# Kernel optimization log

Measured on AMD Instinct MI355X. Metric: run time of the kernel, lower is better.

## Reference

```python
import jax, jax.numpy as jnp
import numpy as np

B, C, H, W = 512, 64, 32, 64
NUM_NODE = 128


def setup_inputs() -> dict:
    key = jax.random.key(0)
    ks = jax.random.split(key, 11)
    f = jnp.float32
    def nrm(k, shape, s):
        return jax.random.normal(k, shape, f) * s
    return {
        "x":   jax.random.normal(ks[0], (B, C, H, W), f),
        "w11": nrm(ks[1], (32, 64, 1, 1), 0.1), "b11": nrm(ks[2], (32,), 0.05),
        "w12": nrm(ks[3], (16, 32, 3, 3), 0.1), "b12": nrm(ks[4], (16,), 0.05),
        "w21": nrm(ks[5], (8, 16, 1, 1), 0.1),  "b21": nrm(ks[6], (8,), 0.05),
        "w22": nrm(ks[7], (4, 8, 3, 3), 0.1),   "b22": nrm(ks[8], (4,), 0.05),
        "fcw": nrm(ks[9], (2 * NUM_NODE, 32 * 64 * 4), 0.05),
        "fcb": nrm(ks[10], (2 * NUM_NODE,), 0.05),
    }


def _conv_relu(x, w, b, pad):
    y = jax.lax.conv_general_dilated(
        x, w, window_strides=(1, 1), padding=[(pad, pad), (pad, pad)],
        dimension_numbers=("NCHW", "OIHW", "NCHW"))
    return jax.nn.relu(y + b[None, :, None, None])


def reference(x, w11, b11, w12, b12, w21, b21, w22, b22, fcw, fcb):
    # --- GraphGen3: conv stack -> fc -> n_Sigmoid -> [B, N, 2] ---
    h = _conv_relu(x, w11, b11, 0)
    h = _conv_relu(h, w12, b12, 1)
    h = _conv_relu(h, w21, b21, 0)
    h = _conv_relu(h, w22, b22, 1)          # [B, 4, 32, 64]
    z = h.reshape(h.shape[0], -1) @ fcw.T + fcb  # [B, 2N]
    c01 = jax.nn.sigmoid(3.0 * z).reshape(x.shape[0], -1, 2)  # n_Sigmoid(x, 3)
    # --- get_coord: scale normalized coords to pixel range ---
    Hd, Wd = x.shape[2], x.shape[3]
    coord = c01 * jnp.array([Hd - 1, Wd - 1], x.dtype)  # [B, N, 2]
    # --- th_batch_map_coordinates: clamp, corner gather, bilinear lerp ---
    ch = jnp.clip(coord[..., 0], 0.0, Hd - 1)
    cw = jnp.clip(coord[..., 1], 0.0, Wd - 1)
    h0 = jnp.floor(ch).astype(jnp.int32); h1 = jnp.ceil(ch).astype(jnp.int32)
    w0 = jnp.floor(cw).astype(jnp.int32); w1 = jnp.ceil(cw).astype(jnp.int32)
    bidx = jnp.arange(x.shape[0])[:, None]  # [B, 1]
    def gv(hi, wi):
        return x[bidx, :, hi, wi]           # gather -> [B, N, C]
    v_lt = gv(h0, w0); v_rt = gv(h1, w0)
    v_lb = gv(h0, w1); v_rb = gv(h1, w1)
    oh = (ch - h0.astype(x.dtype))[..., None]
    ow = (cw - w0.astype(x.dtype))[..., None]
    vt = v_lt + oh * (v_rt - v_lt)
    vb = v_lb + oh * (v_rb - v_lb)
    graph_feat = vt + ow * (vb - vt)        # [B, N, C] (matches permute(0,2,1))
    return graph_feat, coord
```

## Files before the change

kernel.cpp:

```cpp
#include <hip/hip_runtime.h>
#include <cstdint>

#define BATCH 512
#define CIN   64
#define HH    32
#define WW    64
#define HW    2048
#define C1    32
#define C2    16
#define C3    8
#define C4    4
#define NOUT  256
#define KFC   8192
#define NODES 128
#define KS    16
#define GF_SIZE (BATCH * NODES * CIN)

typedef __attribute__((ext_vector_type(8))) short bfrag;
typedef __attribute__((ext_vector_type(4))) float ffrag;

__device__ __forceinline__ ushort bf_trunc(float f) { return (ushort)(__float_as_uint(f) >> 16); }
__device__ __forceinline__ float  bf_truncf(float f) { return __uint_as_float(__float_as_uint(f) & 0xffff0000u); }
__device__ __forceinline__ ushort f2bf(float f) {
  uint32_t u = __float_as_uint(f);
  return (ushort)((u + 0x7fffu + ((u >> 16) & 1u)) >> 16);
}
__device__ __forceinline__ uint32_t pack2(float a, float b) {
  return (uint32_t)f2bf(a) | ((uint32_t)f2bf(b) << 16);
}
__device__ __forceinline__ uint32_t packhi2(float a, float b) {
  return (uint32_t)bf_trunc(a) | ((uint32_t)bf_trunc(b) << 16);
}

__global__ __launch_bounds__(256) void k_conv12(
    const float* __restrict__ x, const float* __restrict__ w11, const float* __restrict__ b11,
    const float* __restrict__ w12, const float* __restrict__ b12,
    float* __restrict__ h2, int b0)
{
  __shared__ __align__(16) char h1s[10 * 66 * 64];
  const int tid = threadIdx.x;
  const int l   = tid & 63;
  const int wv  = tid >> 6;
  const int lr  = l & 15;
  const int lg  = l >> 4;
  const int r0  = blockIdx.x * 8;
  const int bg  = b0 + blockIdx.y;
  const float* xb = x + (size_t)bg * CIN * HW;

  if (tid < 160) {
    int row = tid >> 4, half = (tid >> 3) & 1, q = tid & 7;
    int cell = row * 66 + (half ? 65 : 0);
    *(uint2*)(h1s + (cell << 6) + q * 8) = uint2{0u, 0u};
  }

  bfrag w1h[2][2], w1l[2][2];
  #pragma unroll
  for (int m = 0; m < 2; ++m) {
    #pragma unroll
    for (int ks = 0; ks < 2; ++ks) {
      const float* wp = w11 + (m * 16 + lr) * 64 + ks * 32 + lg * 8;
      #pragma unroll
      for (int e = 0; e < 8; ++e) {
        float v = wp[e];
        w1h[m][ks][e] = (short)bf_trunc(v);
        w1l[m][ks][e] = (short)f2bf(v - bf_truncf(v));
      }
    }
  }
  float bias1[2][4];
  #pragma unroll
  for (int m = 0; m < 2; ++m) {
    #pragma unroll
    for (int r = 0; r < 4; ++r) bias1[m][r] = b11[m * 16 + lg * 4 + r];
  }

  #pragma unroll 2
  for (int i = 0; i < 10; ++i) {
    const int nt   = wv * 10 + i;
    const int ry   = nt >> 2;
    const int col0 = (nt & 3) << 4;
    const int y    = r0 - 1 + ry;
    const int colb = col0 + 1 + lr;
    if (y >= 0 && y < HH) {
      const float* xp = xb + y * WW + col0 + lr;
      bfrag xh[2];
      #pragma unroll
      for (int ks = 0; ks < 2; ++ks) {
        #pragma unroll
        for (int e = 0; e < 8; ++e)
          xh[ks][e] = (short)f2bf(xp[(ks * 32 + lg * 8 + e) * HW]);
      }
      ffrag a0 = {0.f, 0.f, 0.f, 0.f}, a1 = {0.f, 0.f, 0.f, 0.f};
      #pragma unroll
      for (int ks = 0; ks < 2; ++ks) {
        a0 = __builtin_amdgcn_mfma_f32_16x16x32_bf16(w1h[0][ks], xh[ks], a0, 0, 0, 0);
        a0 = __builtin_amdgcn_mfma_f32_16x16x32_bf16(w1l[0][ks], xh[ks], a0, 0, 0, 0);
        a1 = __builtin_amdgcn_mfma_f32_16x16x32_bf16(w1h[1][ks], xh[ks], a1, 0, 0, 0);
        a1 = __builtin_amdgcn_mfma_f32_16x16x32_bf16(w1l[1][ks], xh[ks], a1, 0, 0, 0);
      }
      #pragma unroll
      for (int m = 0; m < 2; ++m) {
        float v0 = fmaxf((m ? a1[0] : a0[0]) + bias1[m][0], 0.f);
        float v1 = fmaxf((m ? a1[1] : a0[1]) + bias1[m][1], 0.f);
        float v2 = fmaxf((m ? a1[2] : a0[2]) + bias1[m][2], 0.f);
        float v3 = fmaxf((m ? a1[3] : a0[3]) + bias1[m][3], 0.f);
        int chunk = (m * 2 + (lg >> 1)) ^ ((colb >> 1) & 3);
        char* dst = h1s + ((ry * 66 + colb) << 6) + (chunk << 4) + (lg & 1) * 8;
        *(uint2*)dst = uint2{pack2(v0, v1), pack2(v2, v3)};
      }
    } else {
      #pragma unroll
      for (int m = 0; m < 2; ++m) {
        int chunk = (m * 2 + (lg >> 1)) ^ ((colb >> 1) & 3);
        char* dst = h1s + ((ry * 66 + colb) << 6) + (chunk << 4) + (lg & 1) * 8;
        *(uint2*)dst = uint2{0u, 0u};
      }
    }
  }
  __syncthreads();

  bfrag w2h[9], w2l[9];
  #pragma unroll
  for (int t = 0; t < 9; ++t) {
    const float* wp = w12 + lr * 288 + t;
    #pragma unroll
    for (int e = 0; e < 8; ++e) {
      float v = wp[(lg * 8 + e) * 9];
      w2h[t][e] = (short)bf_trunc(v);
      w2l[t][e] = (short)f2bf(v - bf_truncf(v));
    }
  }
  float bias2[4];
  #pragma unroll
  for (int r = 0; r < 4; ++r) bias2[r] = b12[lg * 4 + r];

  #pragma unroll 2
  for (int i = 0; i < 8; ++i) {
    const int nt   = wv * 8 + i;
    const int ryo  = nt >> 2;
    const int col0 = (nt & 3) << 4;
    ffrag acc = {0.f, 0.f, 0.f, 0.f};
    #pragma unroll
    for (int ky = 0; ky < 3; ++ky) {
      const int row = ryo + ky;
      #pragma unroll
      for (int kx = 0; kx < 3; ++kx) {
        const int colb  = col0 + lr + kx;
        const int chunk = lg ^ ((colb >> 1) & 3);
        const bfrag hv = *(const bfrag*)(h1s + ((row * 66 + colb) << 6) + (chunk << 4));
        acc = __builtin_amdgcn_mfma_f32_16x16x32_bf16(w2h[ky * 3 + kx], hv, acc, 0, 0, 0);
        acc = __builtin_amdgcn_mfma_f32_16x16x32_bf16(w2l[ky * 3 + kx], hv, acc, 0, 0, 0);
      }
    }
    const int px = (r0 + ryo) * WW + col0 + lr;
    float4 o;
    o.x = fmaxf(acc[0] + bias2[0], 0.f);
    o.y = fmaxf(acc[1] + bias2[1], 0.f);
    o.z = fmaxf(acc[2] + bias2[2], 0.f);
    o.w = fmaxf(acc[3] + bias2[3], 0.f);
    *(float4*)(h2 + ((size_t)blockIdx.y * HW + px) * 16 + lg * 4) = o;
  }
}

__global__ __launch_bounds__(256) void k_conv34(
    const float* __restrict__ h2, const float* __restrict__ w21, const float* __restrict__ b21,
    const float* __restrict__ w22, const float* __restrict__ b22,
    ushort* __restrict__ h4h, ushort* __restrict__ h4l)
{
  __shared__ float h3s[18][64][9];
  __shared__ float __align__(16) w21s[128];
  __shared__ float __align__(16) w22s[288];
  const int tid = threadIdx.x;
  const int r0  = blockIdx.x * 16;
  const size_t b = blockIdx.y;

  for (int i = tid; i < 128; i += 256) w21s[(i & 15) * 8 + (i >> 4)] = w21[i];
  for (int i = tid; i < 288; i += 256) {
    int o = i / 72, r = i - o * 72, c = r / 9, tap = r - c * 9;
    w22s[(tap * 8 + c) * 4 + o] = w22[i];
  }
  __syncthreads();

  for (int p = tid; p < 18 * 64; p += 256) {
    const int ry = p >> 6, wc = p & 63;
    const int y  = r0 - 1 + ry;
    float* hd = &h3s[ry][wc][0];
    if (y >= 0 && y < HH) {
      const float4* hp = (const float4*)(h2 + ((b * HH + y) * WW + wc) * C2);
      float4 v0 = hp[0], v1 = hp[1], v2 = hp[2], v3 = hp[3];
      float xv[16] = {v0.x, v0.y, v0.z, v0.w, v1.x, v1.y, v1.z, v1.w,
                      v2.x, v2.y, v2.z, v2.w, v3.x, v3.y, v3.z, v3.w};
      float acc[C3];
      #pragma unroll
      for (int o = 0; o < C3; ++o) acc[o] = b21[o];
      #pragma unroll
      for (int c = 0; c < 16; ++c) {
        const float4* wr = (const float4*)&w21s[c * 8];
        float4 a = wr[0], d = wr[1];
        float v = xv[c];
        acc[0] = fmaf(v, a.x, acc[0]); acc[1] = fmaf(v, a.y, acc[1]);
        acc[2] = fmaf(v, a.z, acc[2]); acc[3] = fmaf(v, a.w, acc[3]);
        acc[4] = fmaf(v, d.x, acc[4]); acc[5] = fmaf(v, d.y, acc[5]);
        acc[6] = fmaf(v, d.z, acc[6]); acc[7] = fmaf(v, d.w, acc[7]);
      }
      #pragma unroll
      for (int c = 0; c < C3; ++c) hd[c] = fmaxf(acc[c], 0.f);
    } else {
      #pragma unroll
      for (int c = 0; c < C3; ++c) hd[c] = 0.f;
    }
  }
  __syncthreads();

  for (int p = tid; p < 1024; p += 256) {
    const int yl = p >> 6, wc = p & 63, ry = yl + 1;
    float acc[C4] = {b22[0], b22[1], b22[2], b22[3]};
    #pragma unroll
    for (int ky = 0; ky < 3; ++ky) {
      #pragma unroll
      for (int kx = 0; kx < 3; ++kx) {
        const int wcc = wc + kx - 1;
        if (wcc < 0 || wcc >= WW) continue;
        const float* hb = &h3s[ry + ky - 1][wcc][0];
        const int tap = ky * 3 + kx;
        #pragma unroll
        for (int c = 0; c < C3; ++c) {
          float v = hb[c];
          float4 w4 = *(const float4*)&w22s[(tap * 8 + c) * 4];
          acc[0] = fmaf(v, w4.x, acc[0]); acc[1] = fmaf(v, w4.y, acc[1]);
          acc[2] = fmaf(v, w4.z, acc[2]); acc[3] = fmaf(v, w4.w, acc[3]);
        }
      }
    }
    const size_t base = b * KFC + (r0 + yl) * WW + wc;
    #pragma unroll
    for (int o = 0; o < C4; ++o) {
      float v = fmaxf(acc[o], 0.f);
      h4h[base + (size_t)o * HW] = bf_trunc(v);
      h4l[base + (size_t)o * HW] = f2bf(v - bf_truncf(v));
    }
  }
}

__global__ __launch_bounds__(256) void k_cvt_fcw(
    const float* __restrict__ w, ushort* __restrict__ hi, ushort* __restrict__ lo)
{
  const int i = (blockIdx.x * 256 + threadIdx.x) * 8;
  const float4 a = *(const float4*)(w + i);
  const float4 b = *(const float4*)(w + i + 4);
  uint4 hv, lv;
  hv.x = packhi2(a.x, a.y); hv.y = packhi2(a.z, a.w);
  hv.z = packhi2(b.x, b.y); hv.w = packhi2(b.z, b.w);
  lv.x = pack2(a.x - bf_truncf(a.x), a.y - bf_truncf(a.y));
  lv.y = pack2(a.z - bf_truncf(a.z), a.w - bf_truncf(a.w));
  lv.z = pack2(b.x - bf_truncf(b.x), b.y - bf_truncf(b.y));
  lv.w = pack2(b.z - bf_truncf(b.z), b.w - bf_truncf(b.w));
  *(uint4*)(hi + i) = hv;
  *(uint4*)(lo + i) = lv;
}

__global__ __launch_bounds__(256) void k_fc(
    const ushort* __restrict__ Ahp, const ushort* __restrict__ Alp,
    const ushort* __restrict__ Bhp, const ushort* __restrict__ Blp,
    float* __restrict__ zpart, int cb)
{
  const int tid = threadIdx.x;
  const int l   = tid & 63;
  const int wv  = tid >> 6;
  const int lr  = l & 15;
  const int lg  = l >> 4;
  const int m0  = blockIdx.x * 64 + (wv >> 1) * 32;
  const int n0  = blockIdx.y * 64 + (wv & 1) * 32;
  const int k0  = blockIdx.z * (KFC / KS);

  int mrow[2], nrow[2];
  #pragma unroll
  for (int t = 0; t < 2; ++t) {
    int m = m0 + t * 16 + lr;
    mrow[t] = m < cb ? m : cb - 1;
    nrow[t] = n0 + t * 16 + lr;
  }
  ffrag acc[2][2] = {};

  #pragma unroll 1
  for (int kc = 0; kc < (KFC / KS) / 32; ++kc) {
    const int k = k0 + kc * 32 + lg * 8;
    bfrag ah[2], al[2], bh[2], bl[2];
    #pragma unroll
    for (int t = 0; t < 2; ++t) {
      ah[t] = *(const bfrag*)(Ahp + (size_t)mrow[t] * KFC + k);
      al[t] = *(const bfrag*)(Alp + (size_t)mrow[t] * KFC + k);
      bh[t] = *(const bfrag*)(Bhp + (size_t)nrow[t] * KFC + k);
      bl[t] = *(const bfrag*)(Blp + (size_t)nrow[t] * KFC + k);
    }
    #pragma unroll
    for (int mt = 0; mt < 2; ++mt) {
      #pragma unroll
      for (int nt = 0; nt < 2; ++nt) {
        acc[mt][nt] = __builtin_amdgcn_mfma_f32_16x16x32_bf16(ah[mt], bh[nt], acc[mt][nt], 0, 0, 0);
        acc[mt][nt] = __builtin_amdgcn_mfma_f32_16x16x32_bf16(ah[mt], bl[nt], acc[mt][nt], 0, 0, 0);
        acc[mt][nt] = __builtin_amdgcn_mfma_f32_16x16x32_bf16(al[mt], bh[nt], acc[mt][nt], 0, 0, 0);
      }
    }
  }

  #pragma unroll
  for (int mt = 0; mt < 2; ++mt) {
    #pragma unroll
    for (int r = 0; r < 4; ++r) {
      const int m = m0 + mt * 16 + lg * 4 + r;
      if (m < cb) {
        #pragma unroll
        for (int nt = 0; nt < 2; ++nt)
          zpart[((size_t)blockIdx.z * cb + m) * NOUT + n0 + nt * 16 + lr] = acc[mt][nt][r];
      }
    }
  }
}

__global__ __launch_bounds__(256) void k_gather(
    const float* __restrict__ x, const float* __restrict__ zpart,
    const float* __restrict__ fcb, float* __restrict__ out, int cb, int b0)
{
  const int bid = blockIdx.x;
  int bl, g;
  if ((cb & 7) == 0) {
    const int xcd = bid & 7;
    const int j   = bid >> 3;
    g  = j & 31;
    bl = (j >> 5) * 8 + xcd;
  } else {
    bl = bid >> 5;
    g  = bid & 31;
  }
  const int node = g * 4 + (threadIdx.x >> 6);
  const int l    = threadIdx.x & 63;
  const int bg   = b0 + bl;

  float val = 0.f;
  if (l < 2 * KS) {
    const int kb = l >> 1, comp = l & 1;
    val = zpart[((size_t)kb * cb + bl) * NOUT + node * 2 + comp];
  }
  #pragma unroll
  for (int off = 2; off < 2 * KS; off <<= 1) val += __shfl_xor(val, off);
  const float z0 = __shfl(val, 0) + fcb[node * 2 + 0];
  const float z1 = __shfl(val, 1) + fcb[node * 2 + 1];
  const float ch = 31.f / (1.f + __expf(-3.f * z0));
  const float cw = 63.f / (1.f + __expf(-3.f * z1));

  if (l < 2)
    out[GF_SIZE + (((size_t)bg * NODES + node) << 1) + l] = l ? cw : ch;

  const float chv = fminf(fmaxf(ch, 0.f), 31.f);
  const float cwv = fminf(fmaxf(cw, 0.f), 63.f);
  const float fh = floorf(chv), fw = floorf(cwv);
  const int h0 = (int)fh, h1i = (int)ceilf(chv);
  const int w0 = (int)fw, w1i = (int)ceilf(cwv);
  const float oh = chv - fh, ow = cwv - fw;
  const float* xb = x + ((size_t)bg * CIN + l) * HW;
  const float v_lt = xb[h0 * WW + w0];
  const float v_rt = xb[h1i * WW + w0];
  const float v_lb = xb[h0 * WW + w1i];
  const float v_rb = xb[h1i * WW + w1i];
  const float vt = v_lt + oh * (v_rt - v_lt);
  const float vb = v_lb + oh * (v_rb - v_lb);
  out[((size_t)bg * NODES + node) * CIN + l] = vt + ow * (vb - vt);
}

extern "C" void kernel_launch(void* const* d_in, const int* in_sizes, int n_in,
                              void* d_out, int out_size, void* d_ws, size_t ws_size,
                              hipStream_t stream)
{
  (void)in_sizes; (void)n_in; (void)out_size;
  const float* x   = (const float*)d_in[0];
  const float* w11 = (const float*)d_in[1];
  const float* b11 = (const float*)d_in[2];
  const float* w12 = (const float*)d_in[3];
  const float* b12 = (const float*)d_in[4];
  const float* w21 = (const float*)d_in[5];
  const float* b21 = (const float*)d_in[6];
  const float* w22 = (const float*)d_in[7];
  const float* b22 = (const float*)d_in[8];
  const float* fcw = (const float*)d_in[9];
  const float* fcb = (const float*)d_in[10];
  float* out = (float*)d_out;
  char* wsb  = (char*)d_ws;

  const size_t perB  = 131072 + 16384 + 16384 + (size_t)KS * NOUT * 4;
  const size_t fixed = 2 * 4194304;
  size_t avail = ws_size > fixed ? ws_size - fixed : perB;
  size_t cbmax = avail / perB;
  int CB = (int)(cbmax < (size_t)BATCH ? cbmax : (size_t)BATCH);
  if (CB < 1) CB = 1;

  char* p = wsb;
  float*  h2v  = (float*)p;   p += (size_t)CB * 131072;
  ushort* h4h  = (ushort*)p;  p += (size_t)CB * 16384;
  ushort* h4l  = (ushort*)p;  p += (size_t)CB * 16384;
  float*  zpv  = (float*)p;   p += (size_t)CB * KS * NOUT * 4;
  ushort* fcwh = (ushort*)p;  p += 4194304;
  ushort* fcwl = (ushort*)p;

  k_cvt_fcw<<<dim3(NOUT * KFC / (256 * 8)), 256, 0, stream>>>(fcw, fcwh, fcwl);

  for (int b0 = 0; b0 < BATCH; b0 += CB) {
    const int cb = (BATCH - b0 < CB) ? (BATCH - b0) : CB;
    k_conv12<<<dim3(4, cb), 256, 0, stream>>>(x, w11, b11, w12, b12, h2v, b0);
    k_conv34<<<dim3(2, cb), 256, 0, stream>>>(h2v, w21, b21, w22, b22, h4h, h4l);
    k_fc<<<dim3((cb + 63) / 64, 4, KS), 256, 0, stream>>>(h4h, h4l, fcwh, fcwl, zpv, cb);
    k_gather<<<dim3(cb * 32), 256, 0, stream>>>(x, zpv, fcb, out, cb, b0);
  }
}
```

Baseline: 263.1 us.

## Store conv2 output as fp16, halve conv12 row tile, prefetch input tiles

```diff
diff --git a/kernel.cpp b/kernel.cpp
--- a/kernel.cpp
+++ b/kernel.cpp
@@ -1,4 +1,5 @@
 #include <hip/hip_runtime.h>
+#include <hip/hip_fp16.h>
 #include <cstdint>
 
 #define BATCH 512
@@ -31,26 +32,31 @@
 __device__ __forceinline__ uint32_t packhi2(float a, float b) {
   return (uint32_t)bf_trunc(a) | ((uint32_t)bf_trunc(b) << 16);
 }
-
-__global__ __launch_bounds__(256) void k_conv12(
+__device__ __forceinline__ ushort f2h(float f) { return __half_as_ushort(__float2half_rn(f)); }
+__device__ __forceinline__ uint32_t packh2(float a, float b) {
+  return (uint32_t)f2h(a) | ((uint32_t)f2h(b) << 16);
+}
+__device__ __forceinline__ float h2f(uint32_t u) { return __half2float(__ushort_as_half((ushort)u)); }
+
+__global__ __launch_bounds__(256, 5) void k_conv12(
     const float* __restrict__ x, const float* __restrict__ w11, const float* __restrict__ b11,
     const float* __restrict__ w12, const float* __restrict__ b12,
-    float* __restrict__ h2, int b0)
-{
-  __shared__ __align__(16) char h1s[10 * 66 * 64];
+    ushort* __restrict__ h2, int b0)
+{
+  __shared__ __align__(16) char h1s[6 * 66 * 64];
   const int tid = threadIdx.x;
   const int l   = tid & 63;
   const int wv  = tid >> 6;
   const int lr  = l & 15;
   const int lg  = l >> 4;
-  const int r0  = blockIdx.x * 8;
+  const int r0  = blockIdx.x * 4;
   const int bg  = b0 + blockIdx.y;
   const float* xb = x + (size_t)bg * CIN * HW;
 
-  if (tid < 160) {
-    int row = tid >> 4, half = (tid >> 3) & 1, q = tid & 7;
-    int cell = row * 66 + (half ? 65 : 0);
-    *(uint2*)(h1s + (cell << 6) + q * 8) = uint2{0u, 0u};
+  if (tid < 96) {
+    int cell = tid >> 3, q = tid & 7;
+    int row = cell >> 1, colb = (cell & 1) ? 65 : 0;
+    *(uint2*)(h1s + ((row * 66 + colb) << 6) + q * 8) = uint2{0u, 0u};
   }
 
   bfrag w1h[2][2], w1l[2][2];
@@ -74,96 +80,122 @@
     for (int r = 0; r < 4; ++r) bias1[m][r] = b11[m * 16 + lg * 4 + r];
   }
 
-  #pragma unroll 2
-  for (int i = 0; i < 10; ++i) {
-    const int nt   = wv * 10 + i;
-    const int ry   = nt >> 2;
-    const int col0 = (nt & 3) << 4;
-    const int y    = r0 - 1 + ry;
-    const int colb = col0 + 1 + lr;
+  float bufA[16], bufB[16];
+
+  auto loadx16 = [&](int nt, float (&buf)[16]) {
+    const int ry = nt >> 2, col0 = (nt & 3) << 4;
+    const int y  = r0 - 1 + ry;
     if (y >= 0 && y < HH) {
       const float* xp = xb + y * WW + col0 + lr;
-      bfrag xh[2];
-      #pragma unroll
-      for (int ks = 0; ks < 2; ++ks) {
+      #pragma unroll
+      for (int ks = 0; ks < 2; ++ks)
         #pragma unroll
         for (int e = 0; e < 8; ++e)
-          xh[ks][e] = (short)f2bf(xp[(ks * 32 + lg * 8 + e) * HW]);
-      }
-      ffrag a0 = {0.f, 0.f, 0.f, 0.f}, a1 = {0.f, 0.f, 0.f, 0.f};
-      #pragma unroll
-      for (int ks = 0; ks < 2; ++ks) {
-        a0 = __builtin_amdgcn_mfma_f32_16x16x32_bf16(w1h[0][ks], xh[ks], a0, 0, 0, 0);
-        a0 = __builtin_amdgcn_mfma_f32_16x16x32_bf16(w1l[0][ks], xh[ks], a0, 0, 0, 0);
-        a1 = __builtin_amdgcn_mfma_f32_16x16x32_bf16(w1h[1][ks], xh[ks], a1, 0, 0, 0);
-        a1 = __builtin_amdgcn_mfma_f32_16x16x32_bf16(w1l[1][ks], xh[ks], a1, 0, 0, 0);
-      }
-      #pragma unroll
-      for (int m = 0; m < 2; ++m) {
+          buf[ks * 8 + e] = xp[(ks * 32 + lg * 8 + e) * HW];
+    } else {
+      #pragma unroll
+      for (int j = 0; j < 16; ++j) buf[j] = 0.f;
+    }
+  };
+
+  auto comp_tile = [&](int nt, const float (&buf)[16]) {
+    const int ry = nt >> 2, col0 = (nt & 3) << 4;
+    const int y  = r0 - 1 + ry;
+    const bool valid = (y >= 0) && (y < HH);
+    const int colb = col0 + 1 + lr;
+    bfrag xh[2];
+    #pragma unroll
+    for (int ks = 0; ks < 2; ++ks)
+      #pragma unroll
+      for (int e = 0; e < 8; ++e)
+        xh[ks][e] = (short)f2bf(buf[ks * 8 + e]);
+    ffrag a0 = {0.f, 0.f, 0.f, 0.f}, a1 = {0.f, 0.f, 0.f, 0.f};
+    #pragma unroll
+    for (int ks = 0; ks < 2; ++ks) {
+      a0 = __builtin_amdgcn_mfma_f32_16x16x32_bf16(w1h[0][ks], xh[ks], a0, 0, 0, 0);
+      a0 = __builtin_amdgcn_mfma_f32_16x16x32_bf16(w1l[0][ks], xh[ks], a0, 0, 0, 0);
+      a1 = __builtin_amdgcn_mfma_f32_16x16x32_bf16(w1h[1][ks], xh[ks], a1, 0, 0, 0);
+      a1 = __builtin_amdgcn_mfma_f32_16x16x32_bf16(w1l[1][ks], xh[ks], a1, 0, 0, 0);
+    }
+    #pragma unroll
+    for (int m = 0; m < 2; ++m) {
+      uint2 sv;
+      if (valid) {
         float v0 = fmaxf((m ? a1[0] : a0[0]) + bias1[m][0], 0.f);
         float v1 = fmaxf((m ? a1[1] : a0[1]) + bias1[m][1], 0.f);
         float v2 = fmaxf((m ? a1[2] : a0[2]) + bias1[m][2], 0.f);
         float v3 = fmaxf((m ? a1[3] : a0[3]) + bias1[m][3], 0.f);
-        int chunk = (m * 2 + (lg >> 1)) ^ ((colb >> 1) & 3);
-        char* dst = h1s + ((ry * 66 + colb) << 6) + (chunk << 4) + (lg & 1) * 8;
-        *(uint2*)dst = uint2{pack2(v0, v1), pack2(v2, v3)};
-      }
-    } else {
-      #pragma unroll
-      for (int m = 0; m < 2; ++m) {
-        int chunk = (m * 2 + (lg >> 1)) ^ ((colb >> 1) & 3);
-        char* dst = h1s + ((ry * 66 + colb) << 6) + (chunk << 4) + (lg & 1) * 8;
-        *(uint2*)dst = uint2{0u, 0u};
-      }
-    }
+        sv = uint2{pack2(v0, v1), pack2(v2, v3)};
+      } else {
+        sv = uint2{0u, 0u};
+      }
+      int chunk = (m * 2 + (lg >> 1)) ^ ((colb >> 1) & 3);
+      char* dst = h1s + ((ry * 66 + colb) << 6) + (chunk << 4) + (lg & 1) * 8;
+      *(uint2*)dst = sv;
+    }
+  };
+
+  loadx16(wv * 6 + 0, bufA);
+  #pragma unroll
+  for (int i = 0; i < 6; ++i) {
+    if (i < 5) loadx16(wv * 6 + i + 1, (i & 1) ? bufA : bufB);
+    if (i & 1) comp_tile(wv * 6 + i, bufB);
+    else       comp_tile(wv * 6 + i, bufA);
   }
   __syncthreads();
 
-  bfrag w2h[9], w2l[9];
-  #pragma unroll
-  for (int t = 0; t < 9; ++t) {
-    const float* wp = w12 + lr * 288 + t;
-    #pragma unroll
-    for (int e = 0; e < 8; ++e) {
-      float v = wp[(lg * 8 + e) * 9];
-      w2h[t][e] = (short)bf_trunc(v);
-      w2l[t][e] = (short)f2bf(v - bf_truncf(v));
+  ffrag acc2[4] = {{0.f,0.f,0.f,0.f},{0.f,0.f,0.f,0.f},{0.f,0.f,0.f,0.f},{0.f,0.f,0.f,0.f}};
+  #pragma unroll
+  for (int pass = 0; pass < 2; ++pass) {
+    const int t0 = pass ? 5 : 0;
+    const int tn = pass ? 4 : 5;
+    bfrag wh[5], wl[5];
+    #pragma unroll
+    for (int tt = 0; tt < 5; ++tt) {
+      if (tt < tn) {
+        const float* wp = w12 + lr * 288 + (t0 + tt);
+        #pragma unroll
+        for (int e = 0; e < 8; ++e) {
+          float v = wp[(lg * 8 + e) * 9];
+          wh[tt][e] = (short)bf_trunc(v);
+          wl[tt][e] = (short)f2bf(v - bf_truncf(v));
+        }
+      }
+    }
+    #pragma unroll
+    for (int i = 0; i < 4; ++i) {
+      const int nt   = wv * 4 + i;
+      const int ryo  = nt >> 2;
+      const int col0 = (nt & 3) << 4;
+      #pragma unroll
+      for (int tt = 0; tt < 5; ++tt) {
+        if (tt < tn) {
+          const int t = t0 + tt, ky = t / 3, kx = t - ky * 3;
+          const int colb  = col0 + lr + kx;
+          const int chunk = lg ^ ((colb >> 1) & 3);
+          const bfrag hv = *(const bfrag*)(h1s + (((ryo + ky) * 66 + colb) << 6) + (chunk << 4));
+          acc2[i] = __builtin_amdgcn_mfma_f32_16x16x32_bf16(wh[tt], hv, acc2[i], 0, 0, 0);
+          acc2[i] = __builtin_amdgcn_mfma_f32_16x16x32_bf16(wl[tt], hv, acc2[i], 0, 0, 0);
+        }
+      }
     }
   }
   float bias2[4];
   #pragma unroll
   for (int r = 0; r < 4; ++r) bias2[r] = b12[lg * 4 + r];
-
-  #pragma unroll 2
-  for (int i = 0; i < 8; ++i) {
-    const int nt   = wv * 8 + i;
-    const int ryo  = nt >> 2;
-    const int col0 = (nt & 3) << 4;
-    ffrag acc = {0.f, 0.f, 0.f, 0.f};
-    #pragma unroll
-    for (int ky = 0; ky < 3; ++ky) {
-      const int row = ryo + ky;
-      #pragma unroll
-      for (int kx = 0; kx < 3; ++kx) {
-        const int colb  = col0 + lr + kx;
-        const int chunk = lg ^ ((colb >> 1) & 3);
-        const bfrag hv = *(const bfrag*)(h1s + ((row * 66 + colb) << 6) + (chunk << 4));
-        acc = __builtin_amdgcn_mfma_f32_16x16x32_bf16(w2h[ky * 3 + kx], hv, acc, 0, 0, 0);
-        acc = __builtin_amdgcn_mfma_f32_16x16x32_bf16(w2l[ky * 3 + kx], hv, acc, 0, 0, 0);
-      }
-    }
-    const int px = (r0 + ryo) * WW + col0 + lr;
-    float4 o;
-    o.x = fmaxf(acc[0] + bias2[0], 0.f);
-    o.y = fmaxf(acc[1] + bias2[1], 0.f);
-    o.z = fmaxf(acc[2] + bias2[2], 0.f);
-    o.w = fmaxf(acc[3] + bias2[3], 0.f);
-    *(float4*)(h2 + ((size_t)blockIdx.y * HW + px) * 16 + lg * 4) = o;
+  #pragma unroll
+  for (int i = 0; i < 4; ++i) {
+    const int nt   = wv * 4 + i;
+    const int px   = (r0 + (nt >> 2)) * WW + ((nt & 3) << 4) + lr;
+    uint2 o;
+    o.x = packh2(fmaxf(acc2[i][0] + bias2[0], 0.f), fmaxf(acc2[i][1] + bias2[1], 0.f));
+    o.y = packh2(fmaxf(acc2[i][2] + bias2[2], 0.f), fmaxf(acc2[i][3] + bias2[3], 0.f));
+    *(uint2*)(h2 + ((size_t)blockIdx.y * HW + px) * 16 + lg * 4) = o;
   }
 }
 
 __global__ __launch_bounds__(256) void k_conv34(
-    const float* __restrict__ h2, const float* __restrict__ w21, const float* __restrict__ b21,
+    const ushort* __restrict__ h2, const float* __restrict__ w21, const float* __restrict__ b21,
     const float* __restrict__ w22, const float* __restrict__ b22,
     ushort* __restrict__ h4h, ushort* __restrict__ h4l)
 {
@@ -186,10 +218,15 @@
     const int y  = r0 - 1 + ry;
     float* hd = &h3s[ry][wc][0];
     if (y >= 0 && y < HH) {
-      const float4* hp = (const float4*)(h2 + ((b * HH + y) * WW + wc) * C2);
-      float4 v0 = hp[0], v1 = hp[1], v2 = hp[2], v3 = hp[3];
-      float xv[16] = {v0.x, v0.y, v0.z, v0.w, v1.x, v1.y, v1.z, v1.w,
-                      v2.x, v2.y, v2.z, v2.w, v3.x, v3.y, v3.z, v3.w};
+      const uint4* hp = (const uint4*)(h2 + ((b * HH + y) * WW + wc) * 16);
+      uint4 ua = hp[0], ub = hp[1];
+      uint32_t uw[8] = {ua.x, ua.y, ua.z, ua.w, ub.x, ub.y, ub.z, ub.w};
+      float xv[16];
+      #pragma unroll
+      for (int j = 0; j < 8; ++j) {
+        xv[2*j]   = h2f(uw[j] & 0xffffu);
+        xv[2*j+1] = h2f(uw[j] >> 16);
+      }
       float acc[C3];
       #pragma unroll
       for (int o = 0; o < C3; ++o) acc[o] = b21[o];
@@ -358,11 +395,11 @@
   const int h0 = (int)fh, h1i = (int)ceilf(chv);
   const int w0 = (int)fw, w1i = (int)ceilf(cwv);
   const float oh = chv - fh, ow = cwv - fw;
-  const float* xb = x + ((size_t)bg * CIN + l) * HW;
-  const float v_lt = xb[h0 * WW + w0];
-  const float v_rt = xb[h1i * WW + w0];
-  const float v_lb = xb[h0 * WW + w1i];
-  const float v_rb = xb[h1i * WW + w1i];
+  const float* xbp = x + ((size_t)bg * CIN + l) * HW;
+  const float v_lt = xbp[h0 * WW + w0];
+  const float v_rt = xbp[h1i * WW + w0];
+  const float v_lb = xbp[h0 * WW + w1i];
+  const float v_rb = xbp[h1i * WW + w1i];
   const float vt = v_lt + oh * (v_rt - v_lt);
   const float vb = v_lb + oh * (v_rb - v_lb);
   out[((size_t)bg * NODES + node) * CIN + l] = vt + ow * (vb - vt);
@@ -387,7 +424,7 @@
   float* out = (float*)d_out;
   char* wsb  = (char*)d_ws;
 
-  const size_t perB  = 131072 + 16384 + 16384 + (size_t)KS * NOUT * 4;
+  const size_t perB  = 65536 + 16384 + 16384 + (size_t)KS * NOUT * 4;
   const size_t fixed = 2 * 4194304;
   size_t avail = ws_size > fixed ? ws_size - fixed : perB;
   size_t cbmax = avail / perB;
@@ -395,7 +432,7 @@
   if (CB < 1) CB = 1;
 
   char* p = wsb;
-  float*  h2v  = (float*)p;   p += (size_t)CB * 131072;
+  ushort* h2v  = (ushort*)p;  p += (size_t)CB * 65536;
   ushort* h4h  = (ushort*)p;  p += (size_t)CB * 16384;
   ushort* h4l  = (ushort*)p;  p += (size_t)CB * 16384;
   float*  zpv  = (float*)p;   p += (size_t)CB * KS * NOUT * 4;
@@ -406,7 +443,7 @@
 
   for (int b0 = 0; b0 < BATCH; b0 += CB) {
     const int cb = (BATCH - b0 < CB) ? (BATCH - b0) : CB;
-    k_conv12<<<dim3(4, cb), 256, 0, stream>>>(x, w11, b11, w12, b12, h2v, b0);
+    k_conv12<<<dim3(8, cb), 256, 0, stream>>>(x, w11, b11, w12, b12, h2v, b0);
     k_conv34<<<dim3(2, cb), 256, 0, stream>>>(h2v, w21, b21, w22, b22, h4h, h4l);
     k_fc<<<dim3((cb + 63) / 64, 4, KS), 256, 0, stream>>>(h4h, h4l, fcwh, fcwl, zpv, cb);
     k_gather<<<dim3(cb * 32), 256, 0, stream>>>(x, zpv, fcb, out, cb, b0);
```

Result: slower. 352.6 us (+34.0%).

## Pre-transpose input to NHWC bf16, store conv2 output in fp16, prefetch fragments

Applied to the files above, without the earlier changes.

```diff
diff --git a/kernel.cpp b/kernel.cpp
--- a/kernel.cpp
+++ b/kernel.cpp
@@ -1,4 +1,5 @@
 #include <hip/hip_runtime.h>
+#include <hip/hip_fp16.h>
 #include <cstdint>
 
 #define BATCH 512
@@ -31,11 +32,37 @@
 __device__ __forceinline__ uint32_t packhi2(float a, float b) {
   return (uint32_t)bf_trunc(a) | ((uint32_t)bf_trunc(b) << 16);
 }
+__device__ __forceinline__ ushort f2h(float f) { return __half_as_ushort(__float2half_rn(f)); }
+__device__ __forceinline__ uint32_t packh2(float a, float b) {
+  return (uint32_t)f2h(a) | ((uint32_t)f2h(b) << 16);
+}
+__device__ __forceinline__ float h2f(uint32_t u) { return __half2float(__ushort_as_half((ushort)u)); }
+__device__ __forceinline__ float bf2f(ushort u) { return __uint_as_float(((uint32_t)u) << 16); }
+
+__global__ __launch_bounds__(256) void k_xpose(
+    const float* __restrict__ x, ushort* __restrict__ xt)
+{
+  const int b   = blockIdx.y;
+  const int row = blockIdx.x * 4 + (threadIdx.x >> 6);
+  const int px  = threadIdx.x & 63;
+  const float* xp = x + (size_t)b * CIN * HW + row * WW + px;
+  uint32_t packed[32];
+  #pragma unroll
+  for (int c = 0; c < 32; ++c) {
+    float v0 = xp[(size_t)(2 * c) * HW];
+    float v1 = xp[(size_t)(2 * c + 1) * HW];
+    packed[c] = pack2(v0, v1);
+  }
+  ushort* op = xt + ((size_t)b * HW + row * WW + px) * CIN;
+  #pragma unroll
+  for (int q = 0; q < 8; ++q)
+    *(uint4*)(op + q * 8) = *(const uint4*)&packed[q * 4];
+}
 
 __global__ __launch_bounds__(256) void k_conv12(
-    const float* __restrict__ x, const float* __restrict__ w11, const float* __restrict__ b11,
+    const ushort* __restrict__ xt, const float* __restrict__ w11, const float* __restrict__ b11,
     const float* __restrict__ w12, const float* __restrict__ b12,
-    float* __restrict__ h2, int b0)
+    ushort* __restrict__ h2, int b0)
 {
   __shared__ __align__(16) char h1s[10 * 66 * 64];
   const int tid = threadIdx.x;
@@ -45,7 +72,7 @@
   const int lg  = l >> 4;
   const int r0  = blockIdx.x * 8;
   const int bg  = b0 + blockIdx.y;
-  const float* xb = x + (size_t)bg * CIN * HW;
+  const ushort* xtb = xt + (size_t)bg * HW * CIN;
 
   if (tid < 160) {
     int row = tid >> 4, half = (tid >> 3) & 1, q = tid & 7;
@@ -74,47 +101,58 @@
     for (int r = 0; r < 4; ++r) bias1[m][r] = b11[m * 16 + lg * 4 + r];
   }
 
-  #pragma unroll 2
-  for (int i = 0; i < 10; ++i) {
-    const int nt   = wv * 10 + i;
-    const int ry   = nt >> 2;
-    const int col0 = (nt & 3) << 4;
-    const int y    = r0 - 1 + ry;
+  auto ldfrag = [&](int nt, bfrag& f0, bfrag& f1) {
+    const int ry = nt >> 2, col0 = (nt & 3) << 4;
+    const int y  = r0 - 1 + ry;
+    if (y >= 0 && y < HH) {
+      const ushort* xp = xtb + (size_t)(y * WW + col0 + lr) * CIN + lg * 8;
+      f0 = *(const bfrag*)xp;
+      f1 = *(const bfrag*)(xp + 32);
+    } else {
+      #pragma unroll
+      for (int e = 0; e < 8; ++e) { f0[e] = 0; f1[e] = 0; }
+    }
+  };
+  auto comp = [&](int nt, bfrag f0, bfrag f1) {
+    const int ry = nt >> 2, col0 = (nt & 3) << 4;
+    const int y  = r0 - 1 + ry;
+    const bool valid = (y >= 0) && (y < HH);
     const int colb = col0 + 1 + lr;
-    if (y >= 0 && y < HH) {
-      const float* xp = xb + y * WW + col0 + lr;
-      bfrag xh[2];
-      #pragma unroll
-      for (int ks = 0; ks < 2; ++ks) {
-        #pragma unroll
-        for (int e = 0; e < 8; ++e)
-          xh[ks][e] = (short)f2bf(xp[(ks * 32 + lg * 8 + e) * HW]);
-      }
-      ffrag a0 = {0.f, 0.f, 0.f, 0.f}, a1 = {0.f, 0.f, 0.f, 0.f};
-      #pragma unroll
-      for (int ks = 0; ks < 2; ++ks) {
-        a0 = __builtin_amdgcn_mfma_f32_16x16x32_bf16(w1h[0][ks], xh[ks], a0, 0, 0, 0);
-        a0 = __builtin_amdgcn_mfma_f32_16x16x32_bf16(w1l[0][ks], xh[ks], a0, 0, 0, 0);
-        a1 = __builtin_amdgcn_mfma_f32_16x16x32_bf16(w1h[1][ks], xh[ks], a1, 0, 0, 0);
-        a1 = __builtin_amdgcn_mfma_f32_16x16x32_bf16(w1l[1][ks], xh[ks], a1, 0, 0, 0);
-      }
-      #pragma unroll
-      for (int m = 0; m < 2; ++m) {
+    ffrag a0 = {0.f, 0.f, 0.f, 0.f}, a1 = {0.f, 0.f, 0.f, 0.f};
+    a0 = __builtin_amdgcn_mfma_f32_16x16x32_bf16(w1h[0][0], f0, a0, 0, 0, 0);
+    a0 = __builtin_amdgcn_mfma_f32_16x16x32_bf16(w1l[0][0], f0, a0, 0, 0, 0);
+    a0 = __builtin_amdgcn_mfma_f32_16x16x32_bf16(w1h[0][1], f1, a0, 0, 0, 0);
+    a0 = __builtin_amdgcn_mfma_f32_16x16x32_bf16(w1l[0][1], f1, a0, 0, 0, 0);
+    a1 = __builtin_amdgcn_mfma_f32_16x16x32_bf16(w1h[1][0], f0, a1, 0, 0, 0);
+    a1 = __builtin_amdgcn_mfma_f32_16x16x32_bf16(w1l[1][0], f0, a1, 0, 0, 0);
+    a1 = __builtin_amdgcn_mfma_f32_16x16x32_bf16(w1h[1][1], f1, a1, 0, 0, 0);
+    a1 = __builtin_amdgcn_mfma_f32_16x16x32_bf16(w1l[1][1], f1, a1, 0, 0, 0);
+    #pragma unroll
+    for (int m = 0; m < 2; ++m) {
+      uint2 sv;
+      if (valid) {
         float v0 = fmaxf((m ? a1[0] : a0[0]) + bias1[m][0], 0.f);
         float v1 = fmaxf((m ? a1[1] : a0[1]) + bias1[m][1], 0.f);
         float v2 = fmaxf((m ? a1[2] : a0[2]) + bias1[m][2], 0.f);
         float v3 = fmaxf((m ? a1[3] : a0[3]) + bias1[m][3], 0.f);
-        int chunk = (m * 2 + (lg >> 1)) ^ ((colb >> 1) & 3);
-        char* dst = h1s + ((ry * 66 + colb) << 6) + (chunk << 4) + (lg & 1) * 8;
-        *(uint2*)dst = uint2{pack2(v0, v1), pack2(v2, v3)};
-      }
-    } else {
-      #pragma unroll
-      for (int m = 0; m < 2; ++m) {
-        int chunk = (m * 2 + (lg >> 1)) ^ ((colb >> 1) & 3);
-        char* dst = h1s + ((ry * 66 + colb) << 6) + (chunk << 4) + (lg & 1) * 8;
-        *(uint2*)dst = uint2{0u, 0u};
-      }
+        sv = uint2{pack2(v0, v1), pack2(v2, v3)};
+      } else {
+        sv = uint2{0u, 0u};
+      }
+      int chunk = (m * 2 + (lg >> 1)) ^ ((colb >> 1) & 3);
+      char* dst = h1s + ((ry * 66 + colb) << 6) + (chunk << 4) + (lg & 1) * 8;
+      *(uint2*)dst = sv;
+    }
+  };
+
+  {
+    bfrag c0, c1, n0, n1;
+    ldfrag(wv * 10 + 0, c0, c1);
+    #pragma unroll
+    for (int i = 0; i < 10; ++i) {
+      if (i < 9) ldfrag(wv * 10 + i + 1, n0, n1);
+      comp(wv * 10 + i, c0, c1);
+      c0 = n0; c1 = n1;
     }
   }
   __syncthreads();
@@ -153,17 +191,15 @@
       }
     }
     const int px = (r0 + ryo) * WW + col0 + lr;
-    float4 o;
-    o.x = fmaxf(acc[0] + bias2[0], 0.f);
-    o.y = fmaxf(acc[1] + bias2[1], 0.f);
-    o.z = fmaxf(acc[2] + bias2[2], 0.f);
-    o.w = fmaxf(acc[3] + bias2[3], 0.f);
-    *(float4*)(h2 + ((size_t)blockIdx.y * HW + px) * 16 + lg * 4) = o;
+    uint2 o;
+    o.x = packh2(fmaxf(acc[0] + bias2[0], 0.f), fmaxf(acc[1] + bias2[1], 0.f));
+    o.y = packh2(fmaxf(acc[2] + bias2[2], 0.f), fmaxf(acc[3] + bias2[3], 0.f));
+    *(uint2*)(h2 + ((size_t)blockIdx.y * HW + px) * 16 + lg * 4) = o;
   }
 }
 
 __global__ __launch_bounds__(256) void k_conv34(
-    const float* __restrict__ h2, const float* __restrict__ w21, const float* __restrict__ b21,
+    const ushort* __restrict__ h2, const float* __restrict__ w21, const float* __restrict__ b21,
     const float* __restrict__ w22, const float* __restrict__ b22,
     ushort* __restrict__ h4h, ushort* __restrict__ h4l)
 {
@@ -186,10 +222,15 @@
     const int y  = r0 - 1 + ry;
     float* hd = &h3s[ry][wc][0];
     if (y >= 0 && y < HH) {
-      const float4* hp = (const float4*)(h2 + ((b * HH + y) * WW + wc) * C2);
-      float4 v0 = hp[0], v1 = hp[1], v2 = hp[2], v3 = hp[3];
-      float xv[16] = {v0.x, v0.y, v0.z, v0.w, v1.x, v1.y, v1.z, v1.w,
-                      v2.x, v2.y, v2.z, v2.w, v3.x, v3.y, v3.z, v3.w};
+      const uint4* hp = (const uint4*)(h2 + ((b * HH + y) * WW + wc) * 16);
+      uint4 ua = hp[0], ub = hp[1];
+      uint32_t uw[8] = {ua.x, ua.y, ua.z, ua.w, ub.x, ub.y, ub.z, ub.w};
+      float xv[16];
+      #pragma unroll
+      for (int j = 0; j < 8; ++j) {
+        xv[2*j]   = h2f(uw[j] & 0xffffu);
+        xv[2*j+1] = h2f(uw[j] >> 16);
+      }
       float acc[C3];
       #pragma unroll
       for (int o = 0; o < C3; ++o) acc[o] = b21[o];
@@ -319,7 +360,7 @@
 }
 
 __global__ __launch_bounds__(256) void k_gather(
-    const float* __restrict__ x, const float* __restrict__ zpart,
+    const ushort* __restrict__ xt, const float* __restrict__ zpart,
     const float* __restrict__ fcb, float* __restrict__ out, int cb, int b0)
 {
   const int bid = blockIdx.x;
@@ -358,11 +399,11 @@
   const int h0 = (int)fh, h1i = (int)ceilf(chv);
   const int w0 = (int)fw, w1i = (int)ceilf(cwv);
   const float oh = chv - fh, ow = cwv - fw;
-  const float* xb = x + ((size_t)bg * CIN + l) * HW;
-  const float v_lt = xb[h0 * WW + w0];
-  const float v_rt = xb[h1i * WW + w0];
-  const float v_lb = xb[h0 * WW + w1i];
-  const float v_rb = xb[h1i * WW + w1i];
+  const ushort* xbp = xt + (size_t)bg * HW * CIN + l;
+  const float v_lt = bf2f(xbp[(size_t)(h0 * WW + w0) * CIN]);
+  const float v_rt = bf2f(xbp[(size_t)(h1i * WW + w0) * CIN]);
+  const float v_lb = bf2f(xbp[(size_t)(h0 * WW + w1i) * CIN]);
+  const float v_rb = bf2f(xbp[(size_t)(h1i * WW + w1i) * CIN]);
   const float vt = v_lt + oh * (v_rt - v_lt);
   const float vb = v_lb + oh * (v_rb - v_lb);
   out[((size_t)bg * NODES + node) * CIN + l] = vt + ow * (vb - vt);
@@ -387,15 +428,17 @@
   float* out = (float*)d_out;
   char* wsb  = (char*)d_ws;
 
-  const size_t perB  = 131072 + 16384 + 16384 + (size_t)KS * NOUT * 4;
-  const size_t fixed = 2 * 4194304;
+  const size_t xtBytes = (size_t)BATCH * HW * CIN * 2;
+  const size_t perB    = 65536 + 16384 + 16384 + (size_t)KS * NOUT * 4;
+  const size_t fixed   = xtBytes + 2 * 4194304;
   size_t avail = ws_size > fixed ? ws_size - fixed : perB;
   size_t cbmax = avail / perB;
   int CB = (int)(cbmax < (size_t)BATCH ? cbmax : (size_t)BATCH);
   if (CB < 1) CB = 1;
 
   char* p = wsb;
-  float*  h2v  = (float*)p;   p += (size_t)CB * 131072;
+  ushort* xtv  = (ushort*)p;  p += xtBytes;
+  ushort* h2v  = (ushort*)p;  p += (size_t)CB * 65536;
   ushort* h4h  = (ushort*)p;  p += (size_t)CB * 16384;
   ushort* h4l  = (ushort*)p;  p += (size_t)CB * 16384;
   float*  zpv  = (float*)p;   p += (size_t)CB * KS * NOUT * 4;
@@ -403,12 +446,13 @@
   ushort* fcwl = (ushort*)p;
 
   k_cvt_fcw<<<dim3(NOUT * KFC / (256 * 8)), 256, 0, stream>>>(fcw, fcwh, fcwl);
+  k_xpose<<<dim3(8, BATCH), 256, 0, stream>>>(x, xtv);
 
   for (int b0 = 0; b0 < BATCH; b0 += CB) {
     const int cb = (BATCH - b0 < CB) ? (BATCH - b0) : CB;
-    k_conv12<<<dim3(4, cb), 256, 0, stream>>>(x, w11, b11, w12, b12, h2v, b0);
+    k_conv12<<<dim3(4, cb), 256, 0, stream>>>(xtv, w11, b11, w12, b12, h2v, b0);
     k_conv34<<<dim3(2, cb), 256, 0, stream>>>(h2v, w21, b21, w22, b22, h4h, h4l);
     k_fc<<<dim3((cb + 63) / 64, 4, KS), 256, 0, stream>>>(h4h, h4l, fcwh, fcwl, zpv, cb);
-    k_gather<<<dim3(cb * 32), 256, 0, stream>>>(x, zpv, fcb, out, cb, b0);
-  }
-}
+    k_gather<<<dim3(cb * 32), 256, 0, stream>>>(xtv, zpv, fcb, out, cb, b0);
+  }
+}
```

Result: slower. 278.2 us (+5.7%).
